# Optimization experiments

Measured on AMD Instinct MI355X. Metric: run time of the kernel, lower is better.

Reference implementation:

```python
import jax, jax.numpy as jnp
import numpy as np

N = 100000   # nodes
E = 1600000  # edges
D = 128      # in_channels
H = 64       # hidden_channels
G = 64       # graphs in batch
C = 2        # num_classes


def _linear_init(key, fin, fout):
    s = 1.0 / np.sqrt(fin)
    kw, kb = jax.random.split(key)
    w = jax.random.uniform(kw, (fin, fout), jnp.float32, -s, s)
    b = jax.random.uniform(kb, (fout,), jnp.float32, -s, s)
    return w, b


def setup_inputs() -> dict:
    key = jax.random.key(0)
    ks = jax.random.split(key, 12)
    x = jax.random.normal(ks[0], (N, D), jnp.float32)
    edge_index = jax.random.randint(ks[1], (2, E), 0, N)
    batch = jnp.sort(jax.random.randint(ks[2], (N,), 0, G))
    inp = {"x": x, "edge_index": edge_index, "batch": batch}
    fins = [D, H, H]
    for i, fin in enumerate(fins):
        w1, b1 = _linear_init(ks[3 + 2 * i], fin, H)
        w2, b2 = _linear_init(ks[4 + 2 * i], H, H)
        inp[f"l{i}_w1"], inp[f"l{i}_b1"] = w1, b1
        inp[f"l{i}_w2"], inp[f"l{i}_b2"] = w2, b2
    inp["lin1_w"], inp["lin1_b"] = _linear_init(ks[9], H, H)
    inp["lin2_w"], inp["lin2_b"] = _linear_init(ks[10], H, C)
    return inp


def _gin_conv(h, edge_index, w1, b1, w2, b2):
    # sum-aggregate neighbor features: dst += h[src]  (eps = 0)
    agg = jax.ops.segment_sum(h[edge_index[0]], edge_index[1], num_segments=N)
    z = h + agg
    return jnp.maximum(z @ w1 + b1, 0.0) @ w2 + b2


def reference(x, edge_index, batch,
              l0_w1, l0_b1, l0_w2, l0_b2,
              l1_w1, l1_b1, l1_w2, l1_b2,
              l2_w1, l2_b1, l2_w2, l2_b2,
              lin1_w, lin1_b, lin2_w, lin2_b):
    params = [(l0_w1, l0_b1, l0_w2, l0_b2),
              (l1_w1, l1_b1, l1_w2, l1_b2),
              (l2_w1, l2_b1, l2_w2, l2_b2)]
    h = x
    for (w1, b1, w2, b2) in params:
        h = jnp.maximum(_gin_conv(h, edge_index, w1, b1, w2, b2), 0.0)
        # dropout is identity in eval mode
    # global mean pool over graph ids
    sums = jax.ops.segment_sum(h, batch, num_segments=G)          # [G, H]
    cnt = jax.ops.segment_sum(jnp.ones((N,), jnp.float32), batch, num_segments=G)
    pooled = sums / jnp.maximum(cnt, 1.0)[:, None]
    out = jnp.maximum(pooled @ lin1_w + lin1_b, 0.0)
    return out @ lin2_w + lin2_b  # [G, C]
```

## Files before the change

kernel.cpp:

```cpp
#include <hip/hip_runtime.h>
#include <hip/hip_bf16.h>


__device__ inline unsigned short f2bf(float f) {
    union { __hip_bfloat16 b; unsigned short u; } cv;
    cv.b = __float2bfloat16(f);
    return cv.u;
}
__device__ inline float bf2f(unsigned short u) {
    union { __hip_bfloat16 b; unsigned short u16; } cv;
    cv.u16 = u;
    return __bfloat162float(cv.b);
}

__global__ __launch_bounds__(1024) void zero1024_kernel(int* __restrict__ p) {
    p[threadIdx.x] = 0;
}

__global__ __launch_bounds__(256) void count_buckets_kernel(
    const int* __restrict__ ei, int* __restrict__ gcount, int E_) {
    __shared__ int hist[1024];
    const int tid = threadIdx.x;
    for (int i = tid; i < 1024; i += 256) hist[i] = 0;
    __syncthreads();
    const int base = blockIdx.x * 2048;
#pragma unroll
    for (int i = 0; i < 8; i++) {
        int e = base + i * 256 + tid;
        if (e < E_) atomicAdd(&hist[ei[E_ + e] >> 9], 1);
    }
    __syncthreads();
    for (int i = tid; i < 1024; i += 256)
        if (hist[i]) atomicAdd(&gcount[i], hist[i]);
}

__global__ __launch_bounds__(1024) void scan_buckets_kernel(
    const int* __restrict__ gcount, int* __restrict__ bbase,
    int* __restrict__ gcursor, int* __restrict__ rowptr, int K, int E_, int n) {
    __shared__ int sd[1024];
    const int tid = threadIdx.x;
    int v = (tid < K) ? gcount[tid] : 0;
    sd[tid] = v;
    __syncthreads();
    for (int off = 1; off < 1024; off <<= 1) {
        int x = (tid >= off) ? sd[tid - off] : 0;
        __syncthreads();
        sd[tid] += x;
        __syncthreads();
    }
    if (tid < K) {
        int excl = sd[tid] - v;
        bbase[tid] = excl;
        gcursor[tid] = excl;
    }
    if (tid == 0) {
        bbase[K] = E_;
        rowptr[n] = E_;
    }
}

__global__ __launch_bounds__(256) void bucketize_kernel(
    const int* __restrict__ ei, int* __restrict__ gcursor,
    unsigned* __restrict__ bpack, int E_) {
    __shared__ int hist[1024];
    __shared__ int gbase[1024];
    const int tid = threadIdx.x;
    for (int i = tid; i < 1024; i += 256) hist[i] = 0;
    __syncthreads();
    const int base = blockIdx.x * 2048;
    int bkt[8], rnk[8];
    unsigned pk[8];
#pragma unroll
    for (int i = 0; i < 8; i++) {
        int e = base + i * 256 + tid;
        bkt[i] = -1;
        if (e < E_) {
            int s = ei[e];
            int d = ei[E_ + e];
            bkt[i] = d >> 9;
            pk[i] = (unsigned)s | ((unsigned)(d & 511) << 22);
            rnk[i] = atomicAdd(&hist[bkt[i]], 1);
        }
    }
    __syncthreads();
    for (int i = tid; i < 1024; i += 256)
        if (hist[i]) gbase[i] = atomicAdd(&gcursor[i], hist[i]);
    __syncthreads();
#pragma unroll
    for (int i = 0; i < 8; i++)
        if (bkt[i] >= 0) bpack[gbase[bkt[i]] + rnk[i]] = pk[i];
}

__global__ __launch_bounds__(256) void build_csr_kernel(
    const unsigned* __restrict__ bpack, const int* __restrict__ bbase,
    int* __restrict__ rowptr, int* __restrict__ col, int n) {
    __shared__ int cnt[512];
    __shared__ int sp[256];
    const int tid = threadIdx.x;
    const int b = blockIdx.x;
    const int nstart = b << 9;
    const int estart = bbase[b];
    const int eend = bbase[b + 1];
    cnt[tid] = 0;
    cnt[tid + 256] = 0;
    __syncthreads();
    for (int e = estart + tid; e < eend; e += 256)
        atomicAdd(&cnt[bpack[e] >> 22], 1);
    __syncthreads();
    const int v0 = cnt[tid * 2], v1 = cnt[tid * 2 + 1];
    const int s = v0 + v1;
    sp[tid] = s;
    __syncthreads();
    for (int off = 1; off < 256; off <<= 1) {
        int x = (tid >= off) ? sp[tid - off] : 0;
        __syncthreads();
        sp[tid] += x;
        __syncthreads();
    }
    const int excl = sp[tid] - s;
    cnt[tid * 2] = excl;
    cnt[tid * 2 + 1] = excl + v0;
    const int node0 = nstart + tid * 2;
    if (node0 < n) rowptr[node0] = estart + excl;
    if (node0 + 1 < n) rowptr[node0 + 1] = estart + excl + v0;
    __syncthreads();
    for (int e = estart + tid; e < eend; e += 256) {
        unsigned p = bpack[e];
        int pos = estart + atomicAdd(&cnt[p >> 22], 1);
        col[pos] = (int)(p & 0x3FFFFFu);
    }
}

__global__ __launch_bounds__(256) void proj128_kernel(
    const float* __restrict__ x, unsigned short* __restrict__ y,
    const float* __restrict__ w, int n) {
    constexpr int F = 128, STR = F + 2;
    __shared__ float xs[64 * STR];
    const int tid = threadIdx.x;
    const int tile = blockIdx.x;
    for (int idx = tid; idx < 64 * (F / 2); idx += 256) {
        int r = idx >> 6;
        int c = idx & 63;
        int node = tile * 64 + r;
        float2 v = make_float2(0.f, 0.f);
        if (node < n) v = *reinterpret_cast<const float2*>(x + (size_t)node * F + c * 2);
        *reinterpret_cast<float2*>(&xs[r * STR + c * 2]) = v;
    }
    __syncthreads();
    const int lane = tid & 63;
    const int j0 = __builtin_amdgcn_readfirstlane(tid >> 6) << 4;
    float a[16];
#pragma unroll
    for (int jj = 0; jj < 16; jj++) a[jj] = 0.f;
    for (int k = 0; k < F; k += 8) {
        float2 t0 = *reinterpret_cast<const float2*>(&xs[lane * STR + k]);
        float2 t1 = *reinterpret_cast<const float2*>(&xs[lane * STR + k + 2]);
        float2 t2 = *reinterpret_cast<const float2*>(&xs[lane * STR + k + 4]);
        float2 t3 = *reinterpret_cast<const float2*>(&xs[lane * STR + k + 6]);
        const float tv[8] = {t0.x, t0.y, t1.x, t1.y, t2.x, t2.y, t3.x, t3.y};
#pragma unroll
        for (int kk = 0; kk < 8; kk++)
#pragma unroll
            for (int jj = 0; jj < 16; jj++)
                a[jj] = fmaf(tv[kk], w[(k + kk) * 64 + j0 + jj], a[jj]);
    }
    const int node = tile * 64 + lane;
    if (node < n) {
        unsigned pk[8];
#pragma unroll
        for (int jj = 0; jj < 8; jj++)
            pk[jj] = (unsigned)f2bf(a[2 * jj]) | ((unsigned)f2bf(a[2 * jj + 1]) << 16);
        uint4* orow = reinterpret_cast<uint4*>(y + (size_t)node * 64 + j0);
        orow[0] = make_uint4(pk[0], pk[1], pk[2], pk[3]);
        orow[1] = make_uint4(pk[4], pk[5], pk[6], pk[7]);
    }
}

template <bool LAST>
__global__ __launch_bounds__(256) void fused_layer_kernel(
    const unsigned short* __restrict__ yin,
    const int* __restrict__ rowptr, const int* __restrict__ col,
    const float* __restrict__ b1,
    const float* __restrict__ w2, const float* __restrict__ b2,
    const float* __restrict__ w1n,
    unsigned short* __restrict__ yout, float* __restrict__ hout, int n) {
    constexpr int STR = 66;
    __shared__ float tl[64 * STR];
    const int tid = threadIdx.x;
    const int tile = blockIdx.x;
    const int lane = tid & 63;
    const int wv = __builtin_amdgcn_readfirstlane(tid >> 6);
    const float bias1 = b1[lane];

    for (int i = 0; i < 16; ++i) {
        const int node = tile * 64 + wv * 16 + i;
        if (node >= n) break;
        float acc = bf2f(yin[(size_t)node * 64 + lane]);
        const int rs = rowptr[node];
        const int re = rowptr[node + 1];
        int p = rs;
        for (; p + 8 <= re; p += 8) {
            int c0 = col[p + 0], c1 = col[p + 1], c2 = col[p + 2], c3 = col[p + 3];
            int c4 = col[p + 4], c5 = col[p + 5], c6 = col[p + 6], c7 = col[p + 7];
            unsigned short v0 = yin[(size_t)c0 * 64 + lane];
            unsigned short v1 = yin[(size_t)c1 * 64 + lane];
            unsigned short v2 = yin[(size_t)c2 * 64 + lane];
            unsigned short v3 = yin[(size_t)c3 * 64 + lane];
            unsigned short v4 = yin[(size_t)c4 * 64 + lane];
            unsigned short v5 = yin[(size_t)c5 * 64 + lane];
            unsigned short v6 = yin[(size_t)c6 * 64 + lane];
            unsigned short v7 = yin[(size_t)c7 * 64 + lane];
            acc += bf2f(v0); acc += bf2f(v1); acc += bf2f(v2); acc += bf2f(v3);
            acc += bf2f(v4); acc += bf2f(v5); acc += bf2f(v6); acc += bf2f(v7);
        }
        for (; p < re; ++p) acc += bf2f(yin[(size_t)col[p] * 64 + lane]);
        tl[(wv * 16 + i) * STR + lane] = fmaxf(acc + bias1, 0.f);
    }
    __syncthreads();

    const int j0 = wv << 4;
    const int node = tile * 64 + lane;
    float a[16];
#pragma unroll
    for (int jj = 0; jj < 16; jj++) a[jj] = b2[j0 + jj];
    for (int k = 0; k < 64; k += 8) {
        float2 t0 = *reinterpret_cast<const float2*>(&tl[lane * STR + k]);
        float2 t1 = *reinterpret_cast<const float2*>(&tl[lane * STR + k + 2]);
        float2 t2 = *reinterpret_cast<const float2*>(&tl[lane * STR + k + 4]);
        float2 t3 = *reinterpret_cast<const float2*>(&tl[lane * STR + k + 6]);
        const float tv[8] = {t0.x, t0.y, t1.x, t1.y, t2.x, t2.y, t3.x, t3.y};
#pragma unroll
        for (int kk = 0; kk < 8; kk++)
#pragma unroll
            for (int jj = 0; jj < 16; jj++)
                a[jj] = fmaf(tv[kk], w2[(k + kk) * 64 + j0 + jj], a[jj]);
    }
#pragma unroll
    for (int jj = 0; jj < 16; jj++) a[jj] = fmaxf(a[jj], 0.f);

    if (LAST) {
        if (node < n) {
            float* orow = hout + (size_t)node * 64 + j0;
#pragma unroll
            for (int jj = 0; jj < 16; jj += 4) {
                *reinterpret_cast<float4*>(orow + jj) =
                    make_float4(a[jj], a[jj + 1], a[jj + 2], a[jj + 3]);
            }
        }
    } else {
        __syncthreads();
#pragma unroll
        for (int jj = 0; jj < 16; jj++) tl[lane * STR + j0 + jj] = a[jj];
        __syncthreads();
        float a2[16];
#pragma unroll
        for (int jj = 0; jj < 16; jj++) a2[jj] = 0.f;
        for (int k = 0; k < 64; k += 8) {
            float2 t0 = *reinterpret_cast<const float2*>(&tl[lane * STR + k]);
            float2 t1 = *reinterpret_cast<const float2*>(&tl[lane * STR + k + 2]);
            float2 t2 = *reinterpret_cast<const float2*>(&tl[lane * STR + k + 4]);
            float2 t3 = *reinterpret_cast<const float2*>(&tl[lane * STR + k + 6]);
            const float tv[8] = {t0.x, t0.y, t1.x, t1.y, t2.x, t2.y, t3.x, t3.y};
#pragma unroll
            for (int kk = 0; kk < 8; kk++)
#pragma unroll
                for (int jj = 0; jj < 16; jj++)
                    a2[jj] = fmaf(tv[kk], w1n[(k + kk) * 64 + j0 + jj], a2[jj]);
        }
        if (node < n) {
            unsigned pk[8];
#pragma unroll
            for (int jj = 0; jj < 8; jj++)
                pk[jj] = (unsigned)f2bf(a2[2 * jj]) | ((unsigned)f2bf(a2[2 * jj + 1]) << 16);
            uint4* orow = reinterpret_cast<uint4*>(yout + (size_t)node * 64 + j0);
            orow[0] = make_uint4(pk[0], pk[1], pk[2], pk[3]);
            orow[1] = make_uint4(pk[4], pk[5], pk[6], pk[7]);
        }
    }
}

#define POOL_PARTS 16
__global__ __launch_bounds__(256) void pool_partial_kernel(
    const float* __restrict__ h, const int* __restrict__ batch,
    float* __restrict__ partials, int n) {
    const int g = blockIdx.x >> 4;
    const int part = blockIdx.x & 15;
    const int tid = threadIdx.x;
    auto lb = [&](int key) {
        int lo = 0, hi = n;
        while (lo < hi) {
            int mid = (lo + hi) >> 1;
            if (batch[mid] < key) lo = mid + 1;
            else hi = mid;
        }
        return lo;
    };
    const int lo = lb(g), hi = lb(g + 1);
    const int cnt = hi - lo;
    const int s0 = lo + (int)(((long long)cnt * part) / POOL_PARTS);
    const int s1 = lo + (int)(((long long)cnt * (part + 1)) / POOL_PARTS);

    const int f = tid & 63;
    const int q = tid >> 6;
    float s = 0.f;
    for (int i = s0 + q; i < s1; i += 4) s += h[(size_t)i * 64 + f];

    __shared__ float red[256];
    red[tid] = s;
    __syncthreads();
    if (tid < 64) {
        partials[(size_t)blockIdx.x * 64 + tid] =
            red[tid] + red[tid + 64] + red[tid + 128] + red[tid + 192];
    }
}

__global__ __launch_bounds__(64) void pool_head_kernel(
    const float* __restrict__ partials, const int* __restrict__ batch,
    const float* __restrict__ l1w, const float* __restrict__ l1b,
    const float* __restrict__ l2w, const float* __restrict__ l2b,
    float* __restrict__ out, int n) {
    const int g = blockIdx.x;
    const int tid = threadIdx.x;
    auto lb = [&](int key) {
        int lo = 0, hi = n;
        while (lo < hi) {
            int mid = (lo + hi) >> 1;
            if (batch[mid] < key) lo = mid + 1;
            else hi = mid;
        }
        return lo;
    };
    const int cnt = lb(g + 1) - lb(g);

    __shared__ float pooled[64];
    __shared__ float r[64];
    float v = 0.f;
#pragma unroll
    for (int p = 0; p < POOL_PARTS; p++)
        v += partials[(size_t)(g * POOL_PARTS + p) * 64 + tid];
    pooled[tid] = v / (float)((cnt > 1) ? cnt : 1);
    __syncthreads();
    float a = l1b[tid];
    for (int k = 0; k < 64; k++) a = fmaf(pooled[k], l1w[k * 64 + tid], a);
    r[tid] = fmaxf(a, 0.f);
    __syncthreads();
    if (tid < 2) {
        float a2 = l2b[tid];
        for (int k = 0; k < 64; k++) a2 = fmaf(r[k], l2w[k * 2 + tid], a2);
        out[g * 2 + tid] = a2;
    }
}


extern "C" void kernel_launch(void* const* d_in, const int* in_sizes, int n_in,
                              void* d_out, int out_size, void* d_ws, size_t ws_size,
                              hipStream_t stream) {
    const float* x    = (const float*)d_in[0];
    const int* ei     = (const int*)d_in[1];
    const int* batch  = (const int*)d_in[2];
    const float* l0w1 = (const float*)d_in[3];
    const float* l0b1 = (const float*)d_in[4];
    const float* l0w2 = (const float*)d_in[5];
    const float* l0b2 = (const float*)d_in[6];
    const float* l1w1 = (const float*)d_in[7];
    const float* l1b1 = (const float*)d_in[8];
    const float* l1w2 = (const float*)d_in[9];
    const float* l1b2 = (const float*)d_in[10];
    const float* l2w1 = (const float*)d_in[11];
    const float* l2b1 = (const float*)d_in[12];
    const float* l2w2 = (const float*)d_in[13];
    const float* l2b2 = (const float*)d_in[14];
    const float* lin1w = (const float*)d_in[15];
    const float* lin1b = (const float*)d_in[16];
    const float* lin2w = (const float*)d_in[17];
    const float* lin2b = (const float*)d_in[18];
    float* out = (float*)d_out;

    const int N  = in_sizes[2];
    const int E_ = in_sizes[1] / 2;
    const int K  = (N + 511) >> 9;
    const int G  = out_size / 2;

    char* ws = (char*)d_ws;
    size_t off = 0;
    auto alloc = [&](size_t bytes) {
        void* p = ws + off;
        off += (bytes + 255) & ~(size_t)255;
        return p;
    };
    int* rowptr  = (int*)alloc((size_t)(N + 1) * 4);
    int* col     = (int*)alloc((size_t)E_ * 4);
    int* gcount  = (int*)alloc(1024 * 4);
    int* bbase   = (int*)alloc(1025 * 4);
    int* gcursor = (int*)alloc(1024 * 4);
    float* partials = (float*)alloc((size_t)G * POOL_PARTS * 64 * 4);
    unsigned short* yA = (unsigned short*)alloc((size_t)N * 64 * 2);
    unsigned short* yB = (unsigned short*)alloc((size_t)N * 64 * 2);
    float* hbuf  = (float*)alloc((size_t)N * 64 * 4);
    unsigned* bpack = (unsigned*)hbuf;
    (void)ws_size;

    const int nch = (E_ + 2047) / 2048;

    zero1024_kernel<<<1, 1024, 0, stream>>>(gcount);
    count_buckets_kernel<<<nch, 256, 0, stream>>>(ei, gcount, E_);
    scan_buckets_kernel<<<1, 1024, 0, stream>>>(gcount, bbase, gcursor, rowptr, K, E_, N);
    bucketize_kernel<<<nch, 256, 0, stream>>>(ei, gcursor, bpack, E_);
    build_csr_kernel<<<K, 256, 0, stream>>>(bpack, bbase, rowptr, col, N);

    const int ntiles = (N + 63) / 64;

    proj128_kernel<<<ntiles, 256, 0, stream>>>(x, yA, l0w1, N);
    fused_layer_kernel<false><<<ntiles, 256, 0, stream>>>(
        yA, rowptr, col, l0b1, l0w2, l0b2, l1w1, yB, nullptr, N);
    fused_layer_kernel<false><<<ntiles, 256, 0, stream>>>(
        yB, rowptr, col, l1b1, l1w2, l1b2, l2w1, yA, nullptr, N);
    fused_layer_kernel<true><<<ntiles, 256, 0, stream>>>(
        yA, rowptr, col, l2b1, l2w2, l2b2, nullptr, nullptr, hbuf, N);

    pool_partial_kernel<<<G * POOL_PARTS, 256, 0, stream>>>(hbuf, batch, partials, N);
    pool_head_kernel<<<G, 64, 0, stream>>>(partials, batch, lin1w, lin1b, lin2w, lin2b, out, N);
}
```

Measured before the change: 338.4 us.

## Gather neighbor rows as packed bf16 pairs across half-waves, two nodes per iteration

The neighbor-aggregation loop now loads 32-bit words, each holding two bf16 features. Each half-wave handles alternating edges, and two destination nodes are processed together so more gathers are in flight. Partial sums are combined with a cross-half shuffle. The input projection kernel also stores x in shared memory as packed bf16 to halve LDS use, which rounds the input to bf16 before the first GEMM and so lowers precision.

Measured after the change: 310.0 us. 8.4% less time.

```diff
diff --git a/kernel.cpp b/kernel.cpp
--- a/kernel.cpp
+++ b/kernel.cpp
@@ -7,10 +7,11 @@
     cv.b = __float2bfloat16(f);
     return cv.u;
 }
-__device__ inline float bf2f(unsigned short u) {
-    union { __hip_bfloat16 b; unsigned short u16; } cv;
-    cv.u16 = u;
-    return __bfloat162float(cv.b);
+__device__ inline float bflo(unsigned int v) {
+    union { unsigned int u; float f; } c; c.u = v << 16; return c.f;
+}
+__device__ inline float bfhi(unsigned int v) {
+    union { unsigned int u; float f; } c; c.u = v & 0xffff0000u; return c.f;
 }
 
 __global__ __launch_bounds__(1024) void zero1024_kernel(int* __restrict__ p) {
@@ -134,17 +135,17 @@
 __global__ __launch_bounds__(256) void proj128_kernel(
     const float* __restrict__ x, unsigned short* __restrict__ y,
     const float* __restrict__ w, int n) {
-    constexpr int F = 128, STR = F + 2;
-    __shared__ float xs[64 * STR];
+    constexpr int STR = 66;
+    __shared__ unsigned int xs[64 * STR];
     const int tid = threadIdx.x;
     const int tile = blockIdx.x;
-    for (int idx = tid; idx < 64 * (F / 2); idx += 256) {
+    for (int idx = tid; idx < 64 * 64; idx += 256) {
         int r = idx >> 6;
         int c = idx & 63;
         int node = tile * 64 + r;
         float2 v = make_float2(0.f, 0.f);
-        if (node < n) v = *reinterpret_cast<const float2*>(x + (size_t)node * F + c * 2);
-        *reinterpret_cast<float2*>(&xs[r * STR + c * 2]) = v;
+        if (node < n) v = *reinterpret_cast<const float2*>(x + (size_t)node * 128 + c * 2);
+        xs[r * STR + c] = (unsigned)f2bf(v.x) | ((unsigned)f2bf(v.y) << 16);
     }
     __syncthreads();
     const int lane = tid & 63;
@@ -152,12 +153,13 @@
     float a[16];
 #pragma unroll
     for (int jj = 0; jj < 16; jj++) a[jj] = 0.f;
-    for (int k = 0; k < F; k += 8) {
-        float2 t0 = *reinterpret_cast<const float2*>(&xs[lane * STR + k]);
-        float2 t1 = *reinterpret_cast<const float2*>(&xs[lane * STR + k + 2]);
-        float2 t2 = *reinterpret_cast<const float2*>(&xs[lane * STR + k + 4]);
-        float2 t3 = *reinterpret_cast<const float2*>(&xs[lane * STR + k + 6]);
-        const float tv[8] = {t0.x, t0.y, t1.x, t1.y, t2.x, t2.y, t3.x, t3.y};
+    for (int k = 0; k < 128; k += 8) {
+        unsigned p0 = xs[lane * STR + k / 2 + 0];
+        unsigned p1 = xs[lane * STR + k / 2 + 1];
+        unsigned p2 = xs[lane * STR + k / 2 + 2];
+        unsigned p3 = xs[lane * STR + k / 2 + 3];
+        const float tv[8] = {bflo(p0), bfhi(p0), bflo(p1), bfhi(p1),
+                             bflo(p2), bfhi(p2), bflo(p3), bfhi(p3)};
 #pragma unroll
         for (int kk = 0; kk < 8; kk++)
 #pragma unroll
@@ -190,31 +192,62 @@
     const int tile = blockIdx.x;
     const int lane = tid & 63;
     const int wv = __builtin_amdgcn_readfirstlane(tid >> 6);
-    const float bias1 = b1[lane];
-
-    for (int i = 0; i < 16; ++i) {
-        const int node = tile * 64 + wv * 16 + i;
-        if (node >= n) break;
-        float acc = bf2f(yin[(size_t)node * 64 + lane]);
-        const int rs = rowptr[node];
-        const int re = rowptr[node + 1];
-        int p = rs;
-        for (; p + 8 <= re; p += 8) {
-            int c0 = col[p + 0], c1 = col[p + 1], c2 = col[p + 2], c3 = col[p + 3];
-            int c4 = col[p + 4], c5 = col[p + 5], c6 = col[p + 6], c7 = col[p + 7];
-            unsigned short v0 = yin[(size_t)c0 * 64 + lane];
-            unsigned short v1 = yin[(size_t)c1 * 64 + lane];
-            unsigned short v2 = yin[(size_t)c2 * 64 + lane];
-            unsigned short v3 = yin[(size_t)c3 * 64 + lane];
-            unsigned short v4 = yin[(size_t)c4 * 64 + lane];
-            unsigned short v5 = yin[(size_t)c5 * 64 + lane];
-            unsigned short v6 = yin[(size_t)c6 * 64 + lane];
-            unsigned short v7 = yin[(size_t)c7 * 64 + lane];
-            acc += bf2f(v0); acc += bf2f(v1); acc += bf2f(v2); acc += bf2f(v3);
-            acc += bf2f(v4); acc += bf2f(v5); acc += bf2f(v6); acc += bf2f(v7);
-        }
-        for (; p < re; ++p) acc += bf2f(yin[(size_t)col[p] * 64 + lane]);
-        tl[(wv * 16 + i) * STR + lane] = fmaxf(acc + bias1, 0.f);
+    const int sub = lane & 31;
+    const int h = lane >> 5;
+    const unsigned int* y32 = reinterpret_cast<const unsigned int*>(yin);
+    const float2 b1v = *reinterpret_cast<const float2*>(b1 + 2 * sub);
+
+    for (int j = 0; j < 8; ++j) {
+        const int iA = wv * 16 + 2 * j;
+        const int iB = iA + 1;
+        const int nA = tile * 64 + iA;
+        const int nB = nA + 1;
+        int rsA = 0, reA = 0, rsB = 0, reB = 0;
+        if (nA < n) { rsA = rowptr[nA]; reA = rowptr[nA + 1]; }
+        if (nB < n) { rsB = rowptr[nB]; reB = rowptr[nB + 1]; }
+        const int degA = reA - rsA;
+        const int degB = reB - rsB;
+        float2 accA = make_float2(0.f, 0.f);
+        float2 accB = make_float2(0.f, 0.f);
+        {
+            const int sn = h ? nB : nA;
+            unsigned int sv = 0;
+            if (sn < n) sv = y32[(size_t)sn * 32 + sub];
+            const float slo = bflo(sv), shi = bfhi(sv);
+            accA.x += h ? 0.f : slo;  accA.y += h ? 0.f : shi;
+            accB.x += h ? slo : 0.f;  accB.y += h ? shi : 0.f;
+        }
+        const int mdeg = degA > degB ? degA : degB;
+        for (int base = 0; base < mdeg; base += 16) {
+            int ca[8], cb[8];
+#pragma unroll
+            for (int k = 0; k < 8; ++k) {
+                const int q = base + 2 * k + h;
+                ca[k] = (q < degA) ? col[rsA + q] : -1;
+                cb[k] = (q < degB) ? col[rsB + q] : -1;
+            }
+            unsigned int va[8], vb[8];
+#pragma unroll
+            for (int k = 0; k < 8; ++k) {
+                va[k] = (ca[k] >= 0) ? y32[(size_t)ca[k] * 32 + sub] : 0u;
+                vb[k] = (cb[k] >= 0) ? y32[(size_t)cb[k] * 32 + sub] : 0u;
+            }
+#pragma unroll
+            for (int k = 0; k < 8; ++k) {
+                accA.x += bflo(va[k]); accA.y += bfhi(va[k]);
+                accB.x += bflo(vb[k]); accB.y += bfhi(vb[k]);
+            }
+        }
+        accA.x += __shfl_xor(accA.x, 32);
+        accA.y += __shfl_xor(accA.y, 32);
+        accB.x += __shfl_xor(accB.x, 32);
+        accB.y += __shfl_xor(accB.y, 32);
+        const int wi = h ? iB : iA;
+        float2 wv2 = h ? accB : accA;
+        wv2.x = fmaxf(wv2.x + b1v.x, 0.f);
+        wv2.y = fmaxf(wv2.y + b1v.y, 0.f);
+        if (tile * 64 + wi < n)
+            *reinterpret_cast<float2*>(&tl[wi * STR + 2 * sub]) = wv2;
     }
     __syncthreads();
 
```
